# Kernel optimization log

Measured on AMD Instinct MI355X. Metric: run time of the kernel, lower is better.

The kernel has to match this reference:

```python
import jax, jax.numpy as jnp
import numpy as np

N_HEAD = 16
DIM = 1024
DIM_HEAD = DIM // N_HEAD
B, S = 4, 2048


def setup_inputs() -> dict:
    key = jax.random.key(0)
    ks = jax.random.split(key, 12)
    p = lambda k, shape: jax.random.normal(k, shape, dtype=jnp.float32) * 0.02
    return {
        "query": jax.random.normal(ks[0], (B, S, DIM), dtype=jnp.float32),
        "key": jax.random.normal(ks[1], (B, S, DIM), dtype=jnp.float32),
        "value": jax.random.normal(ks[2], (B, S, DIM), dtype=jnp.float32),
        "mask": jnp.zeros((B, 1, S, S), dtype=bool),
        "w_q": p(ks[3], (DIM, DIM)), "b_q": jnp.zeros((DIM,), jnp.float32),
        "w_k": p(ks[4], (DIM, DIM)), "b_k": jnp.zeros((DIM,), jnp.float32),
        "w_v": p(ks[5], (DIM, DIM)), "b_v": jnp.zeros((DIM,), jnp.float32),
        "w_o": p(ks[6], (DIM, DIM)), "b_o": jnp.zeros((DIM,), jnp.float32),
    }


def _split_heads(x):
    b, s, _ = x.shape
    return x.reshape(b, s, N_HEAD, DIM_HEAD).transpose(0, 2, 1, 3)  # [b,h,s,dh]


def reference(query, key, value, mask, w_q, b_q, w_k, b_k, w_v, b_v, w_o, b_o):
    # QKV projections (torch Linear: x @ W^T + b)
    Q = _split_heads(query @ w_q.T + b_q)
    K = _split_heads(key @ w_k.T + b_k)
    V = _split_heads(value @ w_v.T + b_v)
    scale = 1.0 / np.sqrt(DIM_HEAD).astype(np.float32)
    scores = jnp.einsum("bhqd,bhkd->bhqk", Q, K) * scale  # [b,h,sq,sk]
    scores = jnp.where(mask, -jnp.inf, scores)
    probs = jax.nn.softmax(scores, axis=-1)
    attn = jnp.einsum("bhqk,bhkd->bhqd", probs, V)
    b, h, s, dh = attn.shape
    merged = attn.transpose(0, 2, 1, 3).reshape(b, s, h * dh)
    return merged @ w_o.T + b_o
```

## Files before the change

kernel.cpp:

```cpp
#include <hip/hip_runtime.h>
#include <hip/hip_bf16.h>
#include <stdint.h>

#define B_N 4
#define S_N 2048
#define DIM_N 1024
#define H_N 16
#define DH_N 64
#define M_ROWS (B_N * S_N)
#define BH_N (B_N * H_N)
#define C1 0.18033688011112042f

typedef unsigned short u16;
typedef __attribute__((ext_vector_type(8))) short short8;
typedef __attribute__((ext_vector_type(4))) float f32x4;
typedef __attribute__((ext_vector_type(16))) float f32x16;

typedef __attribute__((address_space(1))) const void gvoid_t;
typedef __attribute__((address_space(3))) void lvoid_t;

__device__ __forceinline__ u16 f2bf(float f) {
  union { float f; uint32_t u; } c; c.f = f;
  uint32_t u = c.u;
  return (u16)((u + 0x7FFFu + ((u >> 16) & 1u)) >> 16);
}

__device__ __forceinline__ uint32_t pk2(float lo, float hi) {
  float2 f; f.x = lo; f.y = hi;
  __hip_bfloat162 h = __float22bfloat162_rn(f);
  union { __hip_bfloat162 h; uint32_t u; } c; c.h = h;
  return c.u;
}

__global__ void cvt3_kernel(const float* __restrict__ s0, const float* __restrict__ s1,
                            const float* __restrict__ s2, u16* __restrict__ d0,
                            u16* __restrict__ d1, u16* __restrict__ d2_, int n4) {
  const int y = blockIdx.y;
  const float* s = (y == 0) ? s0 : (y == 1 ? s1 : s2);
  u16* d = (y == 0) ? d0 : (y == 1 ? d1 : d2_);
  int i = blockIdx.x * blockDim.x + threadIdx.x;
  if (i >= n4) return;
  float4 v = reinterpret_cast<const float4*>(s)[i];
  ushort4 o;
  o.x = f2bf(v.x); o.y = f2bf(v.y); o.z = f2bf(v.z); o.w = f2bf(v.w);
  reinterpret_cast<ushort4*>(d)[i] = o;
}

__global__ void cvt4_kernel(const float* __restrict__ s0, const float* __restrict__ s1,
                            const float* __restrict__ s2, const float* __restrict__ s3,
                            u16* __restrict__ d0, u16* __restrict__ d1,
                            u16* __restrict__ d2_, u16* __restrict__ d3, int n4) {
  const int y = blockIdx.y;
  const float* s = (y == 0) ? s0 : (y == 1 ? s1 : (y == 2 ? s2 : s3));
  u16* d = (y == 0) ? d0 : (y == 1 ? d1 : (y == 2 ? d2_ : d3));
  int i = blockIdx.x * blockDim.x + threadIdx.x;
  if (i >= n4) return;
  float4 v = reinterpret_cast<const float4*>(s)[i];
  ushort4 o;
  o.x = f2bf(v.x); o.y = f2bf(v.y); o.z = f2bf(v.z); o.w = f2bf(v.w);
  reinterpret_cast<ushort4*>(d)[i] = o;
}

__global__ void pack_mask(const uint8_t* __restrict__ m, uint32_t* __restrict__ bits, int nwords) {
  int i = blockIdx.x * blockDim.x + threadIdx.x;
  if (i >= nwords) return;
  const uint32_t* p = reinterpret_cast<const uint32_t*>(m) + (size_t)i * 8;
  uint32_t out = 0;
#pragma unroll
  for (int w = 0; w < 8; ++w) {
    uint32_t v = p[w];
    if (v & 0x000000FFu) out |= 1u << (w * 4 + 0);
    if (v & 0x0000FF00u) out |= 1u << (w * 4 + 1);
    if (v & 0x00FF0000u) out |= 1u << (w * 4 + 2);
    if (v & 0xFF000000u) out |= 1u << (w * 4 + 3);
  }
  const int b = i >> 17;
  const int rem = i & 131071;
  const int s = rem >> 6, c = rem & 63;
  bits[((size_t)(b * 64 + c) << 11) + s] = out;
}

__global__ __launch_bounds__(256)
void gemm_qkv(const u16* __restrict__ qb, const u16* __restrict__ kb,
              const u16* __restrict__ vb, const u16* __restrict__ wq,
              const u16* __restrict__ wk, const u16* __restrict__ wv,
              const float* __restrict__ bq, const float* __restrict__ bk,
              const float* __restrict__ bv, u16* __restrict__ Qh,
              u16* __restrict__ Kh, u16* __restrict__ Vt)
{
  __shared__ __align__(16) u16 As[128 * 32];
  __shared__ __align__(16) u16 Bs[128 * 32];
  const int z = blockIdx.z;
  const u16* A  = (z == 0) ? qb : (z == 1 ? kb : vb);
  const u16* Bw = (z == 0) ? wq : (z == 1 ? wk : wv);
  const float* bias = (z == 0) ? bq : (z == 1 ? bk : bv);
  u16* outp = (z == 0) ? Qh : (z == 1 ? Kh : Vt);
  const float scale = (z == 0) ? C1 : 1.0f;

  const int m0 = blockIdx.x * 128, n0 = blockIdx.y * 128;
  const int t = threadIdx.x, w = t >> 6;
  const int l = t & 63, lr = l & 15, lg = l >> 4;
  const int wr = (w >> 1) * 64, wc = (w & 1) * 64;
  const int srow = t >> 2;
  const int skoff = (t & 3) * 8;

  f32x4 acc[4][4] = {};

  for (int k0 = 0; k0 < DIM_N; k0 += 32) {
    __syncthreads();
#pragma unroll
    for (int c = 0; c < 2; ++c) {
      const u16* ga = A  + (size_t)(m0 + c * 64 + srow) * DIM_N + k0 + skoff;
      const u16* gb = Bw + (size_t)(n0 + c * 64 + srow) * DIM_N + k0 + skoff;
      u16* la = &As[(c * 64 + 16 * w) * 32];
      u16* lb = &Bs[(c * 64 + 16 * w) * 32];
      __builtin_amdgcn_global_load_lds((gvoid_t*)ga, (lvoid_t*)la, 16, 0, 0);
      __builtin_amdgcn_global_load_lds((gvoid_t*)gb, (lvoid_t*)lb, 16, 0, 0);
    }
    __syncthreads();

    short8 af[4], bfr[4];
#pragma unroll
    for (int mf = 0; mf < 4; ++mf)
      af[mf] = *reinterpret_cast<const short8*>(&As[(wr + mf * 16 + lr) * 32 + lg * 8]);
#pragma unroll
    for (int nf = 0; nf < 4; ++nf)
      bfr[nf] = *reinterpret_cast<const short8*>(&Bs[(wc + nf * 16 + lr) * 32 + lg * 8]);
#pragma unroll
    for (int mf = 0; mf < 4; ++mf)
#pragma unroll
      for (int nf = 0; nf < 4; ++nf)
        acc[mf][nf] = __builtin_amdgcn_mfma_f32_16x16x32_bf16(af[mf], bfr[nf], acc[mf][nf], 0, 0, 0);
  }

  float bv4[4];
#pragma unroll
  for (int nf = 0; nf < 4; ++nf) bv4[nf] = bias[n0 + wc + nf * 16 + lr];

#pragma unroll
  for (int mf = 0; mf < 4; ++mf)
#pragma unroll
    for (int nf = 0; nf < 4; ++nf)
#pragma unroll
      for (int r = 0; r < 4; ++r) {
        int grow = m0 + wr + mf * 16 + lg * 4 + r;
        int gcol = n0 + wc + nf * 16 + lr;
        float v = (acc[mf][nf][r] + bv4[nf]) * scale;
        int b = grow >> 11, s = grow & 2047;
        int h = gcol >> 6, d = gcol & 63;
        size_t idx;
        if (z < 2) {
          idx = ((size_t)(b * H_N + h) * S_N + s) * DH_N + d;
        } else {
          int sp = ((((s & 15) + 4) & 8) ? (s ^ 12) : s);
          idx = ((size_t)(b * H_N + h) * DH_N + d) * S_N + sp;
        }
        outp[idx] = f2bf(v);
      }
}

__global__ __launch_bounds__(256)
void gemm_out(const u16* __restrict__ A, const u16* __restrict__ Bw,
              const float* __restrict__ bias, float* __restrict__ outp)
{
  __shared__ __align__(16) u16 As[128 * 32];
  __shared__ __align__(16) u16 Bs[128 * 32];
  const int m0 = blockIdx.x * 128, n0 = blockIdx.y * 128;
  const int t = threadIdx.x, w = t >> 6;
  const int l = t & 63, lr = l & 15, lg = l >> 4;
  const int wr = (w >> 1) * 64, wc = (w & 1) * 64;
  const int srow = t >> 2;
  const int skoff = (t & 3) * 8;

  f32x4 acc[4][4] = {};

  for (int k0 = 0; k0 < DIM_N; k0 += 32) {
    __syncthreads();
#pragma unroll
    for (int c = 0; c < 2; ++c) {
      const u16* ga = A  + (size_t)(m0 + c * 64 + srow) * DIM_N + k0 + skoff;
      const u16* gb = Bw + (size_t)(n0 + c * 64 + srow) * DIM_N + k0 + skoff;
      u16* la = &As[(c * 64 + 16 * w) * 32];
      u16* lb = &Bs[(c * 64 + 16 * w) * 32];
      __builtin_amdgcn_global_load_lds((gvoid_t*)ga, (lvoid_t*)la, 16, 0, 0);
      __builtin_amdgcn_global_load_lds((gvoid_t*)gb, (lvoid_t*)lb, 16, 0, 0);
    }
    __syncthreads();

    short8 af[4], bfr[4];
#pragma unroll
    for (int mf = 0; mf < 4; ++mf)
      af[mf] = *reinterpret_cast<const short8*>(&As[(wr + mf * 16 + lr) * 32 + lg * 8]);
#pragma unroll
    for (int nf = 0; nf < 4; ++nf)
      bfr[nf] = *reinterpret_cast<const short8*>(&Bs[(wc + nf * 16 + lr) * 32 + lg * 8]);
#pragma unroll
    for (int mf = 0; mf < 4; ++mf)
#pragma unroll
      for (int nf = 0; nf < 4; ++nf)
        acc[mf][nf] = __builtin_amdgcn_mfma_f32_16x16x32_bf16(af[mf], bfr[nf], acc[mf][nf], 0, 0, 0);
  }

  float bv4[4];
#pragma unroll
  for (int nf = 0; nf < 4; ++nf) bv4[nf] = bias[n0 + wc + nf * 16 + lr];

#pragma unroll
  for (int mf = 0; mf < 4; ++mf)
#pragma unroll
    for (int nf = 0; nf < 4; ++nf)
#pragma unroll
      for (int r = 0; r < 4; ++r) {
        int grow = m0 + wr + mf * 16 + lg * 4 + r;
        int gcol = n0 + wc + nf * 16 + lr;
        outp[(size_t)grow * DIM_N + gcol] = acc[mf][nf][r] + bv4[nf];
      }
}

#define AT_WAVES 4
#define QPW 64
#define KVB 64
#define NCH (S_N / KVB)

__global__ __launch_bounds__(256, 2)
void attn_kernel(const u16* __restrict__ Qh, const u16* __restrict__ Kh,
                 const u16* __restrict__ Vt, const uint32_t* __restrict__ mbits,
                 u16* __restrict__ AO)
{
  __shared__ __align__(16) u16 K_lds[2][KVB * DH_N];
  __shared__ __align__(16) u16 V_lds[2][DH_N * KVB];

  const int t = threadIdx.x;
  const int w = t >> 6, l = t & 63;
  const int l31 = l & 31, hl = l >> 5;
  const int kx = l31 & 7;

  const int bx = blockIdx.x;
  const int bh = (bx & 7) * 8 + (bx >> 3);
  const int b = bh >> 4, h = bh & 15;
  const int q0 = blockIdx.y * (AT_WAVES * QPW) + w * QPW;

  const u16* Qp = Qh + (size_t)bh * S_N * DH_N;
  const u16* Kp = Kh + (size_t)bh * S_N * DH_N;
  const u16* Vp = Vt + (size_t)bh * DH_N * S_N;
  const uint32_t* mq0 = mbits + ((size_t)b << 17) + q0 + l31;
  const uint32_t* mq1 = mq0 + 32;

  short8 qf0[4], qf1[4];
#pragma unroll
  for (int u = 0; u < 4; ++u) {
    qf0[u] = *reinterpret_cast<const short8*>(
        Qp + (size_t)(q0 + l31) * DH_N + u * 16 + hl * 8);
    qf1[u] = *reinterpret_cast<const short8*>(
        Qp + (size_t)(q0 + 32 + l31) * DH_N + u * 16 + hl * 8);
  }

  f32x16 o00 = {}, o01 = {}, o10 = {}, o11 = {};
  float lr0 = 0.f, lr1 = 0.f;

  auto STAGE = [&](int buf, int kc) {
#pragma unroll
    for (int p = 0; p < 2; ++p) {
      const int s = p * 256 + t;
      const int row = s >> 3, up = s & 7, j = up ^ (row & 7);
      const u16* gk = Kp + (size_t)(kc * KVB + row) * DH_N + j * 8;
      const u16* gv = Vp + (size_t)row * S_N + kc * KVB + j * 8;
      u16* lk = &K_lds[buf][(p * 256 + w * 64) * 8];
      u16* lv = &V_lds[buf][(p * 256 + w * 64) * 8];
      __builtin_amdgcn_global_load_lds((gvoid_t*)gk, (lvoid_t*)lk, 16, 0, 0);
      __builtin_amdgcn_global_load_lds((gvoid_t*)gv, (lvoid_t*)lv, 16, 0, 0);
    }
  };

  auto softpv = [&](f32x16& z, uint32_t mw, float& lr,
                    f32x16& oA, f32x16& oB, const short8 vf[2][2]) {
    if (mw) {
#pragma unroll
      for (int r = 0; r < 16; ++r)
        if ((mw >> ((r & 3) + 8 * (r >> 2) + 4 * hl)) & 1) z[r] = -1e30f;
    }

    float p[16];
#pragma unroll
    for (int r = 0; r < 16; ++r) p[r] = __builtin_amdgcn_exp2f(z[r]);
    float a8[8], a4[4];
#pragma unroll
    for (int r = 0; r < 8; ++r) a8[r] = p[2 * r] + p[2 * r + 1];
#pragma unroll
    for (int r = 0; r < 4; ++r) a4[r] = a8[2 * r] + a8[2 * r + 1];
    lr += (a4[0] + a4[1]) + (a4[2] + a4[3]);

    union { uint32_t u[4]; short8 s8; } pf0, pf1;
    pf0.u[0] = pk2(p[0], p[1]);   pf0.u[1] = pk2(p[2], p[3]);
    pf0.u[2] = pk2(p[4], p[5]);   pf0.u[3] = pk2(p[6], p[7]);
    pf1.u[0] = pk2(p[8], p[9]);   pf1.u[1] = pk2(p[10], p[11]);
    pf1.u[2] = pk2(p[12], p[13]); pf1.u[3] = pk2(p[14], p[15]);

    __builtin_amdgcn_s_setprio(1);
    oA = __builtin_amdgcn_mfma_f32_32x32x16_bf16(vf[0][0], pf0.s8, oA, 0, 0, 0);
    oB = __builtin_amdgcn_mfma_f32_32x32x16_bf16(vf[0][1], pf0.s8, oB, 0, 0, 0);
    oA = __builtin_amdgcn_mfma_f32_32x32x16_bf16(vf[1][0], pf1.s8, oA, 0, 0, 0);
    oB = __builtin_amdgcn_mfma_f32_32x32x16_bf16(vf[1][1], pf1.s8, oB, 0, 0, 0);
    __builtin_amdgcn_s_setprio(0);
  };

  auto half = [&](int buf, int hh, uint32_t mwg0, uint32_t mwg1) {
    const int kb = hh * 32;
    short8 kf[4];
#pragma unroll
    for (int u = 0; u < 4; ++u)
      kf[u] = *reinterpret_cast<const short8*>(
          &K_lds[buf][(kb + l31) * DH_N + (((2 * u + hl) ^ kx) * 8)]);

    f32x16 z0 = {}, z1 = {};
    __builtin_amdgcn_s_setprio(1);
    z0 = __builtin_amdgcn_mfma_f32_32x32x16_bf16(kf[0], qf0[0], z0, 0, 0, 0);
    z1 = __builtin_amdgcn_mfma_f32_32x32x16_bf16(kf[0], qf1[0], z1, 0, 0, 0);
    z0 = __builtin_amdgcn_mfma_f32_32x32x16_bf16(kf[1], qf0[1], z0, 0, 0, 0);
    z1 = __builtin_amdgcn_mfma_f32_32x32x16_bf16(kf[1], qf1[1], z1, 0, 0, 0);
    z0 = __builtin_amdgcn_mfma_f32_32x32x16_bf16(kf[2], qf0[2], z0, 0, 0, 0);
    z1 = __builtin_amdgcn_mfma_f32_32x32x16_bf16(kf[2], qf1[2], z1, 0, 0, 0);
    z0 = __builtin_amdgcn_mfma_f32_32x32x16_bf16(kf[3], qf0[3], z0, 0, 0, 0);
    z1 = __builtin_amdgcn_mfma_f32_32x32x16_bf16(kf[3], qf1[3], z1, 0, 0, 0);
    __builtin_amdgcn_s_setprio(0);

    short8 vf[2][2];
#pragma unroll
    for (int ks = 0; ks < 2; ++ks)
#pragma unroll
      for (int nf = 0; nf < 2; ++nf)
        vf[ks][nf] = *reinterpret_cast<const short8*>(
            &V_lds[buf][(nf * 32 + l31) * KVB + (((hh * 4 + ks * 2 + hl) ^ kx) * 8)]);

    softpv(z0, mwg0, lr0, o00, o01, vf);
    softpv(z1, mwg1, lr1, o10, o11, vf);
  };

  STAGE(0, 0);
  __syncthreads();
  int cb = 0;
  for (int kc = 0; kc < NCH; ++kc) {
    uint32_t mw00 = mq0[(size_t)(2 * kc) * S_N];
    uint32_t mw10 = mq1[(size_t)(2 * kc) * S_N];
    uint32_t mw01 = mq0[(size_t)(2 * kc + 1) * S_N];
    uint32_t mw11 = mq1[(size_t)(2 * kc + 1) * S_N];
    if (kc + 1 < NCH) STAGE(cb ^ 1, kc + 1);
    half(cb, 0, mw00, mw10);
    half(cb, 1, mw01, mw11);
    __syncthreads();
    cb ^= 1;
  }

  auto fin = [&](float lr, int qg, const f32x16& oA, const f32x16& oB) {
    float l_tot = lr + __shfl_xor(lr, 32);
    float inv_l = 1.0f / l_tot;
    u16* orow = AO + ((size_t)b * S_N + q0 + qg + l31) * DIM_N + h * DH_N;
#pragma unroll
    for (int gg = 0; gg < 4; ++gg) {
      ushort4 v4;
      v4.x = f2bf(oA[gg * 4 + 0] * inv_l);
      v4.y = f2bf(oA[gg * 4 + 1] * inv_l);
      v4.z = f2bf(oA[gg * 4 + 2] * inv_l);
      v4.w = f2bf(oA[gg * 4 + 3] * inv_l);
      *reinterpret_cast<ushort4*>(orow + gg * 8 + hl * 4) = v4;
      ushort4 w4;
      w4.x = f2bf(oB[gg * 4 + 0] * inv_l);
      w4.y = f2bf(oB[gg * 4 + 1] * inv_l);
      w4.z = f2bf(oB[gg * 4 + 2] * inv_l);
      w4.w = f2bf(oB[gg * 4 + 3] * inv_l);
      *reinterpret_cast<ushort4*>(orow + 32 + gg * 8 + hl * 4) = w4;
    }
  };
  fin(lr0, 0, o00, o01);
  fin(lr1, 32, o10, o11);
}

extern "C" void kernel_launch(void* const* d_in, const int* in_sizes, int n_in,
                              void* d_out, int out_size, void* d_ws, size_t ws_size,
                              hipStream_t stream)
{
  const float*   q_in = (const float*)d_in[0];
  const float*   k_in = (const float*)d_in[1];
  const float*   v_in = (const float*)d_in[2];
  const uint8_t* mask = (const uint8_t*)d_in[3];
  const float*   w_q  = (const float*)d_in[4];
  const float*   b_q  = (const float*)d_in[5];
  const float*   w_k  = (const float*)d_in[6];
  const float*   b_k  = (const float*)d_in[7];
  const float*   w_v  = (const float*)d_in[8];
  const float*   b_v  = (const float*)d_in[9];
  const float*   w_o  = (const float*)d_in[10];
  const float*   b_o  = (const float*)d_in[11];

  char* ws = (char*)d_ws;
  size_t off = 0;
  auto alloc = [&](size_t bytes) -> char* {
    char* p = ws + off;
    off += (bytes + 255) & ~(size_t)255;
    return p;
  };
  const size_t act_b = (size_t)M_ROWS * DIM_N * 2;
  const size_t w_b   = (size_t)DIM_N * DIM_N * 2;
  const int    nmw   = B_N * S_N * (S_N / 32);
  u16* qb  = (u16*)alloc(act_b);
  u16* kb  = (u16*)alloc(act_b);
  u16* vb  = (u16*)alloc(act_b);
  u16* wqb = (u16*)alloc(w_b);
  u16* wkb = (u16*)alloc(w_b);
  u16* wvb = (u16*)alloc(w_b);
  u16* wob = (u16*)alloc(w_b);
  u16* Qh  = (u16*)alloc(act_b);
  u16* Kh  = (u16*)alloc(act_b);
  u16* Vt  = (u16*)alloc(act_b);
  uint32_t* mbits = (uint32_t*)alloc((size_t)nmw * 4);
  u16* AO  = qb;

  const int n4a = M_ROWS * DIM_N / 4;
  const int n4w = DIM_N * DIM_N / 4;
  cvt3_kernel<<<dim3(n4a / 256, 3), 256, 0, stream>>>(q_in, k_in, v_in, qb, kb, vb, n4a);
  cvt4_kernel<<<dim3(n4w / 256, 4), 256, 0, stream>>>(w_q, w_k, w_v, w_o,
                                                      wqb, wkb, wvb, wob, n4w);
  pack_mask<<<nmw / 256, 256, 0, stream>>>(mask, mbits, nmw);

  gemm_qkv<<<dim3(M_ROWS / 128, DIM_N / 128, 3), 256, 0, stream>>>(
      qb, kb, vb, wqb, wkb, wvb, b_q, b_k, b_v, Qh, Kh, Vt);

  attn_kernel<<<dim3(64, 8), 256, 0, stream>>>(Qh, Kh, Vt, mbits, AO);

  gemm_out<<<dim3(M_ROWS / 128, DIM_N / 128), 256, 0, stream>>>(
      AO, wob, b_o, (float*)d_out);
}
```

Before: 230.1 us.

## Split KV range across two wave groups per attention block and merge partials

Doubles the attention block to eight waves, with two groups of four waves each processing half the key/value sequence for the same query rows. Partial output accumulators and row sums from the second group are reduced into the first through shared memory before normalization and store. This raises the number of resident waves to hide latency and shortens each wave's serial loop, at the cost of an LDS reduction, extra barriers and higher per-block resource use.

```diff
diff --git a/kernel.cpp b/kernel.cpp
--- a/kernel.cpp
+++ b/kernel.cpp
@@ -217,28 +217,28 @@
       }
 }
 
-#define AT_WAVES 4
 #define QPW 64
 #define KVB 64
-#define NCH (S_N / KVB)
-
-__global__ __launch_bounds__(256, 2)
+#define NCHH 16
+
+__global__ __launch_bounds__(512, 2)
 void attn_kernel(const u16* __restrict__ Qh, const u16* __restrict__ Kh,
                  const u16* __restrict__ Vt, const uint32_t* __restrict__ mbits,
                  u16* __restrict__ AO)
 {
-  __shared__ __align__(16) u16 K_lds[2][KVB * DH_N];
-  __shared__ __align__(16) u16 V_lds[2][DH_N * KVB];
+  __shared__ __align__(16) u16 smem[2][2][2][KVB * DH_N];
 
   const int t = threadIdx.x;
   const int w = t >> 6, l = t & 63;
   const int l31 = l & 31, hl = l >> 5;
   const int kx = l31 & 7;
+  const int g = w >> 2;
+  const int wq = w & 3;
 
   const int bx = blockIdx.x;
   const int bh = (bx & 7) * 8 + (bx >> 3);
   const int b = bh >> 4, h = bh & 15;
-  const int q0 = blockIdx.y * (AT_WAVES * QPW) + w * QPW;
+  const int q0 = blockIdx.y * 256 + wq * QPW;
 
   const u16* Qp = Qh + (size_t)bh * S_N * DH_N;
   const u16* Kp = Kh + (size_t)bh * S_N * DH_N;
@@ -259,14 +259,16 @@
   float lr0 = 0.f, lr1 = 0.f;
 
   auto STAGE = [&](int buf, int kc) {
+    const int kcg = g * NCHH + kc;
+    const int ts = t & 255;
 #pragma unroll
     for (int p = 0; p < 2; ++p) {
-      const int s = p * 256 + t;
+      const int s = p * 256 + ts;
       const int row = s >> 3, up = s & 7, j = up ^ (row & 7);
-      const u16* gk = Kp + (size_t)(kc * KVB + row) * DH_N + j * 8;
-      const u16* gv = Vp + (size_t)row * S_N + kc * KVB + j * 8;
-      u16* lk = &K_lds[buf][(p * 256 + w * 64) * 8];
-      u16* lv = &V_lds[buf][(p * 256 + w * 64) * 8];
+      const u16* gk = Kp + (size_t)(kcg * KVB + row) * DH_N + j * 8;
+      const u16* gv = Vp + (size_t)row * S_N + kcg * KVB + j * 8;
+      u16* lk = &smem[g][buf][0][(p * 256 + wq * 64) * 8];
+      u16* lv = &smem[g][buf][1][(p * 256 + wq * 64) * 8];
       __builtin_amdgcn_global_load_lds((gvoid_t*)gk, (lvoid_t*)lk, 16, 0, 0);
       __builtin_amdgcn_global_load_lds((gvoid_t*)gv, (lvoid_t*)lv, 16, 0, 0);
     }
@@ -310,7 +312,7 @@
 #pragma unroll
     for (int u = 0; u < 4; ++u)
       kf[u] = *reinterpret_cast<const short8*>(
-          &K_lds[buf][(kb + l31) * DH_N + (((2 * u + hl) ^ kx) * 8)]);
+          &smem[g][buf][0][(kb + l31) * DH_N + (((2 * u + hl) ^ kx) * 8)]);
 
     f32x16 z0 = {}, z1 = {};
     __builtin_amdgcn_s_setprio(1);
@@ -330,7 +332,7 @@
 #pragma unroll
       for (int nf = 0; nf < 2; ++nf)
         vf[ks][nf] = *reinterpret_cast<const short8*>(
-            &V_lds[buf][(nf * 32 + l31) * KVB + (((hh * 4 + ks * 2 + hl) ^ kx) * 8)]);
+            &smem[g][buf][1][(nf * 32 + l31) * KVB + (((hh * 4 + ks * 2 + hl) ^ kx) * 8)]);
 
     softpv(z0, mwg0, lr0, o00, o01, vf);
     softpv(z1, mwg1, lr1, o10, o11, vf);
@@ -339,40 +341,69 @@
   STAGE(0, 0);
   __syncthreads();
   int cb = 0;
-  for (int kc = 0; kc < NCH; ++kc) {
-    uint32_t mw00 = mq0[(size_t)(2 * kc) * S_N];
-    uint32_t mw10 = mq1[(size_t)(2 * kc) * S_N];
-    uint32_t mw01 = mq0[(size_t)(2 * kc + 1) * S_N];
-    uint32_t mw11 = mq1[(size_t)(2 * kc + 1) * S_N];
-    if (kc + 1 < NCH) STAGE(cb ^ 1, kc + 1);
+  for (int kc = 0; kc < NCHH; ++kc) {
+    const int c2 = (g * NCHH + kc) * 2;
+    uint32_t mw00 = mq0[(size_t)c2 * S_N];
+    uint32_t mw10 = mq1[(size_t)c2 * S_N];
+    uint32_t mw01 = mq0[(size_t)(c2 + 1) * S_N];
+    uint32_t mw11 = mq1[(size_t)(c2 + 1) * S_N];
+    if (kc + 1 < NCHH) STAGE(cb ^ 1, kc + 1);
     half(cb, 0, mw00, mw10);
     half(cb, 1, mw01, mw11);
     __syncthreads();
     cb ^= 1;
   }
 
-  auto fin = [&](float lr, int qg, const f32x16& oA, const f32x16& oB) {
-    float l_tot = lr + __shfl_xor(lr, 32);
-    float inv_l = 1.0f / l_tot;
-    u16* orow = AO + ((size_t)b * S_N + q0 + qg + l31) * DIM_N + h * DH_N;
-#pragma unroll
-    for (int gg = 0; gg < 4; ++gg) {
-      ushort4 v4;
-      v4.x = f2bf(oA[gg * 4 + 0] * inv_l);
-      v4.y = f2bf(oA[gg * 4 + 1] * inv_l);
-      v4.z = f2bf(oA[gg * 4 + 2] * inv_l);
-      v4.w = f2bf(oA[gg * 4 + 3] * inv_l);
-      *reinterpret_cast<ushort4*>(orow + gg * 8 + hl * 4) = v4;
-      ushort4 w4;
-      w4.x = f2bf(oB[gg * 4 + 0] * inv_l);
-      w4.y = f2bf(oB[gg * 4 + 1] * inv_l);
-      w4.z = f2bf(oB[gg * 4 + 2] * inv_l);
-      w4.w = f2bf(oB[gg * 4 + 3] * inv_l);
-      *reinterpret_cast<ushort4*>(orow + 32 + gg * 8 + hl * 4) = w4;
-    }
-  };
-  fin(lr0, 0, o00, o01);
-  fin(lr1, 32, o10, o11);
+  float* mb = (float*)&smem[0][0][0][0];
+  const int widx = wq * 64 + l;
+  if (g == 1) {
+    float* d = mb + widx * 34;
+    d[0] = lr0; d[1] = lr1;
+#pragma unroll
+    for (int r = 0; r < 16; ++r) { d[2 + r] = o00[r]; d[18 + r] = o01[r]; }
+  }
+  __syncthreads();
+  if (g == 0) {
+    const float* d = mb + widx * 34;
+    lr0 += d[0]; lr1 += d[1];
+#pragma unroll
+    for (int r = 0; r < 16; ++r) { o00[r] += d[2 + r]; o01[r] += d[18 + r]; }
+  }
+  __syncthreads();
+  if (g == 1) {
+    float* d = mb + widx * 32;
+#pragma unroll
+    for (int r = 0; r < 16; ++r) { d[r] = o10[r]; d[16 + r] = o11[r]; }
+  }
+  __syncthreads();
+  if (g == 0) {
+    const float* d = mb + widx * 32;
+#pragma unroll
+    for (int r = 0; r < 16; ++r) { o10[r] += d[r]; o11[r] += d[16 + r]; }
+
+    auto fin = [&](float lr, int qg, const f32x16& oA, const f32x16& oB) {
+      float l_tot = lr + __shfl_xor(lr, 32);
+      float inv_l = 1.0f / l_tot;
+      u16* orow = AO + ((size_t)b * S_N + q0 + qg + l31) * DIM_N + h * DH_N;
+#pragma unroll
+      for (int gg = 0; gg < 4; ++gg) {
+        ushort4 v4;
+        v4.x = f2bf(oA[gg * 4 + 0] * inv_l);
+        v4.y = f2bf(oA[gg * 4 + 1] * inv_l);
+        v4.z = f2bf(oA[gg * 4 + 2] * inv_l);
+        v4.w = f2bf(oA[gg * 4 + 3] * inv_l);
+        *reinterpret_cast<ushort4*>(orow + gg * 8 + hl * 4) = v4;
+        ushort4 w4;
+        w4.x = f2bf(oB[gg * 4 + 0] * inv_l);
+        w4.y = f2bf(oB[gg * 4 + 1] * inv_l);
+        w4.z = f2bf(oB[gg * 4 + 2] * inv_l);
+        w4.w = f2bf(oB[gg * 4 + 3] * inv_l);
+        *reinterpret_cast<ushort4*>(orow + 32 + gg * 8 + hl * 4) = w4;
+      }
+    };
+    fin(lr0, 0, o00, o01);
+    fin(lr1, 32, o10, o11);
+  }
 }
 
 extern "C" void kernel_launch(void* const* d_in, const int* in_sizes, int n_in,
@@ -425,7 +456,7 @@
   gemm_qkv<<<dim3(M_ROWS / 128, DIM_N / 128, 3), 256, 0, stream>>>(
       qb, kb, vb, wqb, wkb, wvb, b_q, b_k, b_v, Qh, Kh, Vt);
 
-  attn_kernel<<<dim3(64, 8), 256, 0, stream>>>(Qh, Kh, Vt, mbits, AO);
+  attn_kernel<<<dim3(64, 8), 512, 0, stream>>>(Qh, Kh, Vt, mbits, AO);
 
   gemm_out<<<dim3(M_ROWS / 128, DIM_N / 128), 256, 0, stream>>>(
       AO, wob, b_o, (float*)d_out);
```

Result: slower. 235.8 us (+2.5%).
